# Optimization experiments

Measured on AMD Instinct MI355X. Metric: run time of the kernel, lower is better.

The kernel has to match this reference:

```python
import jax, jax.numpy as jnp
import numpy as np

Q_SCALE = 255.0 / 32.0  # quantization scale used before phi


def setup_inputs() -> dict:
    key = jax.random.key(0)
    ks = jax.random.split(key, 7)
    B, H, W = 8, 384, 384
    PHI, RHO = 32, 64
    x = jax.random.uniform(ks[0], (B, 1, H, W), jnp.float32)
    # Linear weights stored as [in, out]; scaled like torch default init ~1/sqrt(fan_in)
    w1 = jax.random.normal(ks[1], (1, PHI), jnp.float32) * 1.0
    b1 = jax.random.normal(ks[2], (PHI,), jnp.float32) * 0.1
    w2 = jax.random.normal(ks[3], (PHI, PHI), jnp.float32) * (1.0 / np.sqrt(PHI))
    b2 = jax.random.normal(ks[4], (PHI,), jnp.float32) * 0.1
    w3 = jax.random.normal(ks[5], (PHI, RHO), jnp.float32) * (1.0 / np.sqrt(PHI))
    b3 = jax.random.normal(ks[6], (RHO,), jnp.float32) * 0.1
    return {"x": x, "w1": w1, "b1": b1, "w2": w2, "b2": b2, "w3": w3, "b3": b3}


def _extract_3x3(x):
    # x: [B,1,H,W] -> [B,H,W,9] neighborhoods (zero-padded), matching F.unfold(k=3, pad=1)
    B, _, H, W = x.shape
    xp = jnp.pad(x, ((0, 0), (0, 0), (1, 1), (1, 1)))
    return jnp.stack([xp[:, 0, i:i + H, j:j + W] for i in range(3) for j in range(3)], axis=-1)


def reference(x, w1, b1, w2, b2, w3, b3):
    patches = _extract_3x3(x)                       # [B,H,W,9]
    q = jnp.floor(patches * Q_SCALE)                # quantize
    # phi: Linear(1,PHI) + ReLU + Linear(PHI,PHI)
    h = jax.nn.relu(q[..., None] * w1[0] + b1)      # [B,H,W,9,PHI]
    h = jnp.einsum('bhwnc,cd->bhwnd', h, w2) + b2   # [B,H,W,9,PHI]
    agg = h.mean(axis=3)                            # mean over 9 neighbors -> [B,H,W,PHI]
    # rho: Linear(PHI,RHO) + ReLU
    out = jax.nn.relu(jnp.einsum('bhwc,cd->bhwd', agg, w3) + b3)  # [B,H,W,RHO]
    return out.transpose(0, 3, 1, 2)                # [B,RHO,H,W] (fold with k=1 is a reshape)
```

## Files before the change

### kernel.cpp

```cpp
#include <hip/hip_runtime.h>
#include <math.h>

#define Q_SCALE (255.0f / 32.0f)
#define PHI 32
#define RHO 64
#define HH 384
#define WW 384
#define BB 8
#define RPB 4
#define QPB (WW / 4)
#define QSTRIDE (WW + 8)

__global__ __launch_bounds__(512) void build_table_kernel(
    const float* __restrict__ w1, const float* __restrict__ b1,
    const float* __restrict__ w2, const float* __restrict__ b2,
    const float* __restrict__ w3, float* __restrict__ T) {
    __shared__ float h2[8][PHI];
    const int t = threadIdx.x;
    if (t < 256) {
        const int v = t >> 5, c = t & 31;
        float acc = b2[c];
#pragma unroll
        for (int k = 0; k < PHI; ++k) {
            float h1 = fmaxf((float)v * w1[k] + b1[k], 0.0f);
            acc += h1 * w2[k * PHI + c];
        }
        h2[v][c] = acc;
    }
    __syncthreads();
    {
        const int v = t >> 6, r = t & 63;
        float acc = 0.0f;
#pragma unroll
        for (int c = 0; c < PHI; ++c) acc += h2[v][c] * w3[c * RHO + r];
        T[v * RHO + r] = acc * (1.0f / 9.0f);
    }
}

__global__ __launch_bounds__(RPB * QPB) void deepset_quad_kernel(
    const float* __restrict__ x, const float* __restrict__ Tg,
    const float* __restrict__ b3, float* __restrict__ out) {
    __shared__ unsigned int qe[RPB + 2][QSTRIDE];
    __shared__ float Tl[RHO * 8];
    __shared__ float b3l[RHO];

    const int tid = threadIdx.x;
    const int blk = blockIdx.x;
    const int b = blk / (HH / RPB);
    const int h0 = (blk % (HH / RPB)) * RPB;

    for (int i = tid; i < 8 * RHO; i += RPB * QPB) {
        const int v = i >> 6, r = i & 63;
        Tl[r * 8 + v] = Tg[i];
    }
    if (tid < RHO) b3l[tid] = b3[tid];

    const float* xb = x + (size_t)b * HH * WW;
    {
        const int w = tid;
#pragma unroll
        for (int rr = 0; rr < RPB + 2; ++rr) {
            const int hh = h0 - 1 + rr;
            unsigned int qv = 1u;
            if (hh >= 0 && hh < HH) {
                const float xv = xb[hh * WW + w];
                int q = (int)floorf(xv * Q_SCALE);
                q = q < 0 ? 0 : (q > 7 ? 7 : q);
                qv = 1u << (4 * q);
            }
            qe[rr][w + 1] = qv;
        }
        if (w == 0) {
#pragma unroll
            for (int rr = 0; rr < RPB + 2; ++rr) {
                qe[rr][0] = 1u;
                qe[rr][WW + 1] = 1u;
            }
        }
    }
    __syncthreads();

    const int row = tid / QPB;
    const int qd = tid % QPB;

    unsigned int cs[6];
#pragma unroll
    for (int j = 0; j < 6; ++j)
        cs[j] = qe[row][4 * qd + j] + qe[row + 1][4 * qd + j] + qe[row + 2][4 * qd + j];

    const unsigned int cnt0 = cs[0] + cs[1] + cs[2];
    const unsigned int cnt1 = cs[1] + cs[2] + cs[3];
    const unsigned int cnt2 = cs[2] + cs[3] + cs[4];
    const unsigned int cnt3 = cs[3] + cs[4] + cs[5];

    float c0[8], c1[8], c2[8], c3[8];
#pragma unroll
    for (int v = 0; v < 8; ++v) {
        c0[v] = (float)((cnt0 >> (4 * v)) & 15u);
        c1[v] = (float)((cnt1 >> (4 * v)) & 15u);
        c2[v] = (float)((cnt2 >> (4 * v)) & 15u);
        c3[v] = (float)((cnt3 >> (4 * v)) & 15u);
    }

    float* op = out + ((size_t)b * RHO * HH + (h0 + row)) * WW + 4 * qd;
    const size_t rstride = (size_t)HH * WW;
#pragma unroll 8
    for (int r = 0; r < RHO; ++r) {
        const float4 t0 = *(const float4*)&Tl[r * 8];
        const float4 t1 = *(const float4*)&Tl[r * 8 + 4];
        const float bb = b3l[r];
        float a0 = bb, a1 = bb, a2 = bb, a3 = bb;
        a0 += c0[0] * t0.x + c0[1] * t0.y + c0[2] * t0.z + c0[3] * t0.w;
        a0 += c0[4] * t1.x + c0[5] * t1.y + c0[6] * t1.z + c0[7] * t1.w;
        a1 += c1[0] * t0.x + c1[1] * t0.y + c1[2] * t0.z + c1[3] * t0.w;
        a1 += c1[4] * t1.x + c1[5] * t1.y + c1[6] * t1.z + c1[7] * t1.w;
        a2 += c2[0] * t0.x + c2[1] * t0.y + c2[2] * t0.z + c2[3] * t0.w;
        a2 += c2[4] * t1.x + c2[5] * t1.y + c2[6] * t1.z + c2[7] * t1.w;
        a3 += c3[0] * t0.x + c3[1] * t0.y + c3[2] * t0.z + c3[3] * t0.w;
        a3 += c3[4] * t1.x + c3[5] * t1.y + c3[6] * t1.z + c3[7] * t1.w;
        float4 o;
        o.x = fmaxf(a0, 0.0f);
        o.y = fmaxf(a1, 0.0f);
        o.z = fmaxf(a2, 0.0f);
        o.w = fmaxf(a3, 0.0f);
        *(float4*)op = o;
        op += rstride;
    }
}

extern "C" void kernel_launch(void* const* d_in, const int* in_sizes, int n_in,
                              void* d_out, int out_size, void* d_ws, size_t ws_size,
                              hipStream_t stream) {
    const float* x  = (const float*)d_in[0];
    const float* w1 = (const float*)d_in[1];
    const float* b1 = (const float*)d_in[2];
    const float* w2 = (const float*)d_in[3];
    const float* b2 = (const float*)d_in[4];
    const float* w3 = (const float*)d_in[5];
    const float* b3 = (const float*)d_in[6];
    float* out = (float*)d_out;
    float* T   = (float*)d_ws;

    build_table_kernel<<<1, 512, 0, stream>>>(w1, b1, w2, b2, w3, T);
    deepset_quad_kernel<<<BB * (HH / RPB), RPB * QPB, 0, stream>>>(x, T, b3, out);
}
```

Baseline: 321.2 us.

## Fuse table build into main kernel and use nontemporal output stores

```diff
diff --git a/kernel.cpp b/kernel.cpp
--- a/kernel.cpp
+++ b/kernel.cpp
@@ -9,51 +9,26 @@
 #define BB 8
 #define RPB 4
 #define QPB (WW / 4)
+#define NTHR (RPB * QPB)
 #define QSTRIDE (WW + 8)
 
-__global__ __launch_bounds__(512) void build_table_kernel(
+typedef float f32x4 __attribute__((ext_vector_type(4)));
+
+__global__ __launch_bounds__(NTHR) void deepset_fused_kernel(
+    const float* __restrict__ x,
     const float* __restrict__ w1, const float* __restrict__ b1,
     const float* __restrict__ w2, const float* __restrict__ b2,
-    const float* __restrict__ w3, float* __restrict__ T) {
+    const float* __restrict__ w3, const float* __restrict__ b3,
+    float* __restrict__ out) {
     __shared__ float h2[8][PHI];
-    const int t = threadIdx.x;
-    if (t < 256) {
-        const int v = t >> 5, c = t & 31;
-        float acc = b2[c];
-#pragma unroll
-        for (int k = 0; k < PHI; ++k) {
-            float h1 = fmaxf((float)v * w1[k] + b1[k], 0.0f);
-            acc += h1 * w2[k * PHI + c];
-        }
-        h2[v][c] = acc;
-    }
-    __syncthreads();
-    {
-        const int v = t >> 6, r = t & 63;
-        float acc = 0.0f;
-#pragma unroll
-        for (int c = 0; c < PHI; ++c) acc += h2[v][c] * w3[c * RHO + r];
-        T[v * RHO + r] = acc * (1.0f / 9.0f);
-    }
-}
-
-__global__ __launch_bounds__(RPB * QPB) void deepset_quad_kernel(
-    const float* __restrict__ x, const float* __restrict__ Tg,
-    const float* __restrict__ b3, float* __restrict__ out) {
-    __shared__ unsigned int qe[RPB + 2][QSTRIDE];
     __shared__ float Tl[RHO * 8];
     __shared__ float b3l[RHO];
+    __shared__ unsigned int qe[RPB + 2][QSTRIDE];
 
     const int tid = threadIdx.x;
     const int blk = blockIdx.x;
     const int b = blk / (HH / RPB);
     const int h0 = (blk % (HH / RPB)) * RPB;
-
-    for (int i = tid; i < 8 * RHO; i += RPB * QPB) {
-        const int v = i >> 6, r = i & 63;
-        Tl[r * 8 + v] = Tg[i];
-    }
-    if (tid < RHO) b3l[tid] = b3[tid];
 
     const float* xb = x + (size_t)b * HH * WW;
     {
@@ -78,11 +53,32 @@
             }
         }
     }
+
+    if (tid < 256) {
+        const int v = tid >> 5, c = tid & 31;
+        float acc = b2[c];
+#pragma unroll
+        for (int k = 0; k < PHI; ++k) {
+            float h1 = fmaxf((float)v * w1[k] + b1[k], 0.0f);
+            acc += h1 * w2[k * PHI + c];
+        }
+        h2[v][c] = acc;
+    }
+    __syncthreads();
+
+#pragma unroll
+    for (int i = tid; i < 8 * RHO; i += NTHR) {
+        const int v = i >> 6, r = i & 63;
+        float acc = 0.0f;
+#pragma unroll
+        for (int c = 0; c < PHI; ++c) acc += h2[v][c] * w3[c * RHO + r];
+        Tl[r * 8 + v] = acc * (1.0f / 9.0f);
+    }
+    if (tid < RHO) b3l[tid] = b3[tid];
     __syncthreads();
 
     const int row = tid / QPB;
     const int qd = tid % QPB;
-
     unsigned int cs[6];
 #pragma unroll
     for (int j = 0; j < 6; ++j)
@@ -104,7 +100,7 @@
 
     float* op = out + ((size_t)b * RHO * HH + (h0 + row)) * WW + 4 * qd;
     const size_t rstride = (size_t)HH * WW;
-#pragma unroll 8
+#pragma unroll 4
     for (int r = 0; r < RHO; ++r) {
         const float4 t0 = *(const float4*)&Tl[r * 8];
         const float4 t1 = *(const float4*)&Tl[r * 8 + 4];
@@ -118,12 +114,12 @@
         a2 += c2[4] * t1.x + c2[5] * t1.y + c2[6] * t1.z + c2[7] * t1.w;
         a3 += c3[0] * t0.x + c3[1] * t0.y + c3[2] * t0.z + c3[3] * t0.w;
         a3 += c3[4] * t1.x + c3[5] * t1.y + c3[6] * t1.z + c3[7] * t1.w;
-        float4 o;
-        o.x = fmaxf(a0, 0.0f);
-        o.y = fmaxf(a1, 0.0f);
-        o.z = fmaxf(a2, 0.0f);
-        o.w = fmaxf(a3, 0.0f);
-        *(float4*)op = o;
+        f32x4 o;
+        o[0] = fmaxf(a0, 0.0f);
+        o[1] = fmaxf(a1, 0.0f);
+        o[2] = fmaxf(a2, 0.0f);
+        o[3] = fmaxf(a3, 0.0f);
+        __builtin_nontemporal_store(o, (f32x4*)op);
         op += rstride;
     }
 }
@@ -139,8 +135,7 @@
     const float* w3 = (const float*)d_in[5];
     const float* b3 = (const float*)d_in[6];
     float* out = (float*)d_out;
-    float* T   = (float*)d_ws;
 
-    build_table_kernel<<<1, 512, 0, stream>>>(w1, b1, w2, b2, w3, T);
-    deepset_quad_kernel<<<BB * (HH / RPB), RPB * QPB, 0, stream>>>(x, T, b3, out);
+    deepset_fused_kernel<<<BB * (HH / RPB), NTHR, 0, stream>>>(
+        x, w1, b1, w2, b2, w3, b3, out);
 }
```

After: 315.4 us. Within noise of the previous version (-1.8%).
